# Performance work log

Hardware: AMD Instinct MI355X
Metric: run time of the kernel (lower is better)

The kernel has to match this reference:

```python
import jax, jax.numpy as jnp
import numpy as np

IMG = 224
PS = 16
G = IMG // PS          # 14
P = G * G              # 196 patches
CIN = 3
COUT = 768
B = 64


def setup_inputs() -> dict:
    key = jax.random.key(0)
    k1, k2, k3 = jax.random.split(key, 3)
    x = jax.random.normal(k1, (B, CIN, IMG, IMG), dtype=jnp.float32)
    # per-patch conv kernels, stacked: [P, COUT, CIN, PS, PS]
    W = jax.random.normal(k2, (P, COUT, CIN, PS, PS), dtype=jnp.float32) * 0.02
    b = jax.random.normal(k3, (P, COUT), dtype=jnp.float32) * 0.02
    return {"x": x, "W": W, "b": b}


def reference(x, W, b):
    # Each patch (i,j) is convolved with its own kernel at stride=PS -> a single
    # 1x1 output per patch == dot(patch_pixels, kernel). Batched as one einsum.
    Bn = x.shape[0]
    # [B, C, G, PS, G, PS] -> [B, G, G, C, PS, PS] -> [B, P, C*PS*PS]
    patches = x.reshape(Bn, CIN, G, PS, G, PS).transpose(0, 2, 4, 1, 3, 5)
    patches = patches.reshape(Bn, P, CIN * PS * PS)
    Wm = W.reshape(P, COUT, CIN * PS * PS)
    # [B, P, COUT]
    out = jnp.einsum('bpk,pok->bpo', patches, Wm) + b[None]
    # torch code cats along dim=2 (row-major patch order) then reshapes to
    # [B, COUT, G, G]; row-major patch order matches this reshape exactly.
    return out.transpose(0, 2, 1).reshape(Bn, COUT, G, G)
```

## Files before the change

kernel.cpp:

```cpp
#include <hip/hip_runtime.h>
#include <hip/hip_bf16.h>

#define IMG   224
#define PS    16
#define GDIM  14
#define NPATCH 196
#define CIN   3
#define NCOUT 768
#define NB    64
#define KDIM  768

#define BK    64
#define BN    128
#define LDA   72

using short8  = __attribute__((ext_vector_type(8))) short;
using floatx4 = __attribute__((ext_vector_type(4))) float;

static __device__ __forceinline__ uint2 pk4(float4 v) {
    __hip_bfloat162 lo = __float22bfloat162_rn(make_float2(v.x, v.y));
    __hip_bfloat162 hi = __float22bfloat162_rn(make_float2(v.z, v.w));
    uint2 r;
    r.x = *reinterpret_cast<unsigned int*>(&lo);
    r.y = *reinterpret_cast<unsigned int*>(&hi);
    return r;
}

__global__ __launch_bounds__(256)
void dynconv_gemm(const float* __restrict__ x,
                  const float* __restrict__ W,
                  const float* __restrict__ bias,
                  __hip_bfloat16* __restrict__ ws,
                  float* __restrict__ out,
                  int use_ws) {
    __shared__ __align__(16) short As[NB][LDA];
    __shared__ __align__(16) short Bs[BN][LDA];

    const int tid = threadIdx.x;
    const int p   = blockIdx.x / 6;
    const int no  = blockIdx.x % 6;
    const int o0  = no * BN;

    const int gi = p / GDIM;
    const int gj = p % GDIM;

    const int lane = tid & 63;
    const int wv   = tid >> 6;
    const int row  = lane & 15;
    const int quad = lane >> 4;

    floatx4 acc[4][2] = {};

    const int c4 = (tid & 15) << 2;
    const int rb = tid >> 4;

    const float* Wp = W + ((size_t)p * NCOUT + o0) * KDIM;

    float4 ra[4];
    float4 rbv[8];

    auto loadA = [&](int kk) {
        const int kg  = kk + c4;
        const int ch  = kg >> 8;
        const int rem = kg & 255;
        const int rowoff = (gi * PS + (rem >> 4)) * IMG + gj * PS + (rem & 15);
        #pragma unroll
        for (int i = 0; i < 4; ++i) {
            const int m = rb + (i << 4);
            ra[i] = *(const float4*)(x + (size_t)(m * CIN + ch) * (IMG * IMG) + rowoff);
        }
    };
    auto loadB = [&](int kk) {
        const float* wsrc = Wp + kk + c4;
        #pragma unroll
        for (int i = 0; i < 8; ++i)
            rbv[i] = *(const float4*)(wsrc + (size_t)(rb + (i << 4)) * KDIM);
    };

    loadA(0);
    loadB(0);

    for (int kk = 0; kk < KDIM; kk += BK) {
        __syncthreads();

        #pragma unroll
        for (int i = 0; i < 4; ++i)
            *(uint2*)&As[rb + (i << 4)][c4] = pk4(ra[i]);
        #pragma unroll
        for (int i = 0; i < 8; ++i)
            *(uint2*)&Bs[rb + (i << 4)][c4] = pk4(rbv[i]);

        if (kk + BK < KDIM) {
            loadA(kk + BK);
            loadB(kk + BK);
        }

        __syncthreads();

        #pragma unroll
        for (int ks = 0; ks < 2; ++ks) {
            short8 a[4], bf[2];
            const int kofs = ks * 32 + quad * 8;
            #pragma unroll
            for (int mt = 0; mt < 4; ++mt)
                a[mt] = *(const short8*)&As[mt * 16 + row][kofs];
            #pragma unroll
            for (int nt = 0; nt < 2; ++nt)
                bf[nt] = *(const short8*)&Bs[wv * 32 + nt * 16 + row][kofs];
            #pragma unroll
            for (int mt = 0; mt < 4; ++mt)
                #pragma unroll
                for (int nt = 0; nt < 2; ++nt)
                    acc[mt][nt] = __builtin_amdgcn_mfma_f32_16x16x32_bf16(
                        a[mt], bf[nt], acc[mt][nt], 0, 0, 0);
        }
    }

    #pragma unroll
    for (int mt = 0; mt < 4; ++mt) {
        #pragma unroll
        for (int nt = 0; nt < 2; ++nt) {
            const int n = wv * 32 + nt * 16 + row;
            const int o = o0 + n;
            const float bv = bias[p * NCOUT + o];
            #pragma unroll
            for (int r = 0; r < 4; ++r) {
                const int m = mt * 16 + quad * 4 + r;
                const float val = acc[mt][nt][r] + bv;
                if (use_ws) {
                    ws[((size_t)m * NPATCH + p) * NCOUT + o] = __float2bfloat16(val);
                } else {
                    out[((size_t)m * NCOUT + o) * NPATCH + p] = val;
                }
            }
        }
    }
}

__global__ __launch_bounds__(256)
void dynconv_transpose(const __hip_bfloat16* __restrict__ ws,
                       float* __restrict__ out) {
    __shared__ float tile[32][65];
    const int b  = blockIdx.z;
    const int p0 = blockIdx.x * 32;
    const int o0 = blockIdx.y * 64;
    const int tid = threadIdx.x;

    {
        const int cc = tid & 31;
        const int rr = tid >> 5;
        #pragma unroll
        for (int i = 0; i < 4; ++i) {
            const int pr = p0 + rr + i * 8;
            if (pr < NPATCH) {
                const __hip_bfloat162 v = *(const __hip_bfloat162*)
                    &ws[((size_t)b * NPATCH + pr) * NCOUT + o0 + 2 * cc];
                tile[rr + i * 8][2 * cc]     = __bfloat162float(v.x);
                tile[rr + i * 8][2 * cc + 1] = __bfloat162float(v.y);
            }
        }
    }
    __syncthreads();
    {
        const int c = tid & 31;
        const int r = tid >> 5;
        const int pc = p0 + c;
        if (pc < NPATCH) {
            #pragma unroll
            for (int i = 0; i < 8; ++i) {
                const int orow = o0 + r + i * 8;
                out[((size_t)b * NCOUT + orow) * NPATCH + pc] = tile[c][r + i * 8];
            }
        }
    }
}

extern "C" void kernel_launch(void* const* d_in, const int* in_sizes, int n_in,
                              void* d_out, int out_size, void* d_ws, size_t ws_size,
                              hipStream_t stream) {
    const float* x    = (const float*)d_in[0];
    const float* W    = (const float*)d_in[1];
    const float* bias = (const float*)d_in[2];
    float* out = (float*)d_out;

    const size_t need = (size_t)NB * NPATCH * NCOUT * sizeof(__hip_bfloat16);
    const int use_ws = (d_ws != nullptr && ws_size >= need) ? 1 : 0;
    __hip_bfloat16* ws = (__hip_bfloat16*)d_ws;

    dynconv_gemm<<<dim3(NPATCH * 6), dim3(256), 0, stream>>>(
        x, W, bias, ws, out, use_ws);

    if (use_ws) {
        dynconv_transpose<<<dim3(7, 12, 64), dim3(256), 0, stream>>>(ws, out);
    }
}
```

Measured before the change: 659.0 us.

## Double-buffer LDS tiles with smaller K step and group patches in block order

Switches the GEMM main loop to double-buffered shared-memory tiles, so the next tile's global loads and LDS stores overlap the current MFMA work with one barrier per iteration instead of two. The K step is halved, which shrinks register staging and keeps LDS usage about the same despite two buffers. Block indexing is remapped so eight consecutive patches share a group across the six output-channel slices, with a padded grid and early exit for out-of-range patches. The intent is to hide load latency; the cost is more loop iterations and barriers, each with less MFMA work.

```diff
diff --git a/kernel.cpp b/kernel.cpp
--- a/kernel.cpp
+++ b/kernel.cpp
@@ -10,9 +10,10 @@
 #define NB    64
 #define KDIM  768
 
-#define BK    64
+#define BK    32
 #define BN    128
-#define LDA   72
+#define LDA   40
+#define NITER (KDIM / BK)
 
 using short8  = __attribute__((ext_vector_type(8))) short;
 using floatx4 = __attribute__((ext_vector_type(4))) float;
@@ -33,12 +34,17 @@
                   __hip_bfloat16* __restrict__ ws,
                   float* __restrict__ out,
                   int use_ws) {
-    __shared__ __align__(16) short As[NB][LDA];
-    __shared__ __align__(16) short Bs[BN][LDA];
+    __shared__ __align__(16) short As[2][NB][LDA];
+    __shared__ __align__(16) short Bs[2][BN][LDA];
 
     const int tid = threadIdx.x;
-    const int p   = blockIdx.x / 6;
-    const int no  = blockIdx.x % 6;
+
+    const int id  = blockIdx.x;
+    const int pg  = id / 48;
+    const int rm  = id % 48;
+    const int no  = rm >> 3;
+    const int p   = pg * 8 + (rm & 7);
+    if (p >= NPATCH) return;
     const int o0  = no * BN;
 
     const int gi = p / GDIM;
@@ -51,62 +57,65 @@
 
     floatx4 acc[4][2] = {};
 
-    const int c4 = (tid & 15) << 2;
-    const int rb = tid >> 4;
+    const int c2   = (tid & 7) << 2;
+    const int rowb = tid >> 3;
 
     const float* Wp = W + ((size_t)p * NCOUT + o0) * KDIM;
 
-    float4 ra[4];
-    float4 rbv[8];
+    float4 ra[2];
+    float4 rbv[4];
 
     auto loadA = [&](int kk) {
-        const int kg  = kk + c4;
+        const int kg  = kk + c2;
         const int ch  = kg >> 8;
         const int rem = kg & 255;
         const int rowoff = (gi * PS + (rem >> 4)) * IMG + gj * PS + (rem & 15);
         #pragma unroll
-        for (int i = 0; i < 4; ++i) {
-            const int m = rb + (i << 4);
+        for (int i = 0; i < 2; ++i) {
+            const int m = rowb + (i << 5);
             ra[i] = *(const float4*)(x + (size_t)(m * CIN + ch) * (IMG * IMG) + rowoff);
         }
     };
     auto loadB = [&](int kk) {
-        const float* wsrc = Wp + kk + c4;
-        #pragma unroll
-        for (int i = 0; i < 8; ++i)
-            rbv[i] = *(const float4*)(wsrc + (size_t)(rb + (i << 4)) * KDIM);
+        const float* wsrc = Wp + kk + c2;
+        #pragma unroll
+        for (int i = 0; i < 4; ++i)
+            rbv[i] = *(const float4*)(wsrc + (size_t)(rowb + (i << 5)) * KDIM);
+    };
+    auto storeLDS = [&](int buf) {
+        #pragma unroll
+        for (int i = 0; i < 2; ++i)
+            *(uint2*)&As[buf][rowb + (i << 5)][c2] = pk4(ra[i]);
+        #pragma unroll
+        for (int i = 0; i < 4; ++i)
+            *(uint2*)&Bs[buf][rowb + (i << 5)][c2] = pk4(rbv[i]);
     };
 
     loadA(0);
     loadB(0);
-
-    for (int kk = 0; kk < KDIM; kk += BK) {
+    storeLDS(0);
+
+    for (int it = 0; it < NITER; ++it) {
+        const int cur = it & 1;
+        const int nxt = cur ^ 1;
+        const bool more = (it + 1) < NITER;
+
         __syncthreads();
 
-        #pragma unroll
-        for (int i = 0; i < 4; ++i)
-            *(uint2*)&As[rb + (i << 4)][c4] = pk4(ra[i]);
-        #pragma unroll
-        for (int i = 0; i < 8; ++i)
-            *(uint2*)&Bs[rb + (i << 4)][c4] = pk4(rbv[i]);
-
-        if (kk + BK < KDIM) {
-            loadA(kk + BK);
-            loadB(kk + BK);
-        }
-
-        __syncthreads();
-
-        #pragma unroll
-        for (int ks = 0; ks < 2; ++ks) {
+        if (more) {
+            loadA((it + 1) * BK);
+            loadB((it + 1) * BK);
+        }
+
+        {
             short8 a[4], bf[2];
-            const int kofs = ks * 32 + quad * 8;
+            const int kofs = quad * 8;
             #pragma unroll
             for (int mt = 0; mt < 4; ++mt)
-                a[mt] = *(const short8*)&As[mt * 16 + row][kofs];
+                a[mt] = *(const short8*)&As[cur][mt * 16 + row][kofs];
             #pragma unroll
             for (int nt = 0; nt < 2; ++nt)
-                bf[nt] = *(const short8*)&Bs[wv * 32 + nt * 16 + row][kofs];
+                bf[nt] = *(const short8*)&Bs[cur][wv * 32 + nt * 16 + row][kofs];
             #pragma unroll
             for (int mt = 0; mt < 4; ++mt)
                 #pragma unroll
@@ -114,6 +123,9 @@
                     acc[mt][nt] = __builtin_amdgcn_mfma_f32_16x16x32_bf16(
                         a[mt], bf[nt], acc[mt][nt], 0, 0, 0);
         }
+
+        if (more)
+            storeLDS(nxt);
     }
 
     #pragma unroll
@@ -187,7 +199,7 @@
     const int use_ws = (d_ws != nullptr && ws_size >= need) ? 1 : 0;
     __hip_bfloat16* ws = (__hip_bfloat16*)d_ws;
 
-    dynconv_gemm<<<dim3(NPATCH * 6), dim3(256), 0, stream>>>(
+    dynconv_gemm<<<dim3(1200), dim3(256), 0, stream>>>(
         x, W, bias, ws, out, use_ws);
 
     if (use_ws) {
```

Result: slower. 716.3 us (+8.7%).
